# Performance work log

Measured on AMD Instinct MI355X. Metric: run time of the kernel, lower is better.

## Reference

```python
import jax, jax.numpy as jnp
import numpy as np

EPS = 1e-6

def _exp_map0(v):
    # v: [..., D] tangent at origin with v[...,0]==0
    sp = v[..., 1:]
    n = jnp.sqrt(jnp.clip(jnp.sum(sp * sp, -1, keepdims=True), EPS))
    return jnp.concatenate([jnp.cosh(n), jnp.sinh(n) / n * sp], -1)

def _log_map0(x):
    x0 = x[..., :1]
    sp = x[..., 1:]
    n = jnp.sqrt(jnp.clip(jnp.sum(sp * sp, -1, keepdims=True), EPS))
    d = jnp.arccosh(jnp.clip(x0, 1.0 + EPS))
    return jnp.concatenate([jnp.zeros_like(x0), d / n * sp], -1)

def _pt_to_origin(x, v):
    # parallel transport v from T_x to T_o, o=(1,0,...,0):
    # PT(v) = v + <o,v>_L / (1 - <x,o>_L) * (x + o);  <o,v>_L=-v0, <x,o>_L=-x0
    coef = -v[..., :1] / (1.0 + x[..., :1])
    x_plus_o = jnp.concatenate([x[..., :1] + 1.0, x[..., 1:]], -1)
    return v + coef * x_plus_o

def _linear(h, W, b):
    # torch nn.Linear: h @ W.T + b, W: [out, in]
    return jnp.einsum('bne,de->bnd', h, W) + b

def setup_inputs() -> dict:
    key = jax.random.key(0)
    ks = jax.random.split(key, 8)
    B, N, d = 8, 2048, 256
    # manifold points via exp_map0 of small tangents
    t = jax.random.normal(ks[0], (B, N, d), jnp.float32) * 0.1
    x = _exp_map0(jnp.pad(t, ((0, 0), (0, 0), (1, 0))))
    # tangent velocity at x: project random u onto T_x (add <x,u>_L * x since <x,x>_L=-1)
    u = jax.random.normal(ks[1], (B, N, d + 1), jnp.float32) * 0.1
    xu = jnp.sum(x * u, -1, keepdims=True) - 2.0 * x[..., :1] * u[..., :1]  # Lorentz inner
    x_vel = u + xu * x
    s = 1.0 / np.sqrt(d)
    Wq = jax.random.normal(ks[2], (d, d), jnp.float32) * s
    Wk = jax.random.normal(ks[3], (d, d), jnp.float32) * s
    Wv = jax.random.normal(ks[4], (d, d), jnp.float32) * s
    bq = jnp.zeros((d,), jnp.float32)
    bk = jnp.zeros((d,), jnp.float32)
    bv = jnp.zeros((d,), jnp.float32)
    tau = jnp.ones((1,), jnp.float32)
    return {"x": x, "x_vel": x_vel, "Wq": Wq, "bq": bq, "Wk": Wk, "bk": bk,
            "Wv": Wv, "bv": bv, "tau": tau}

def reference(x, x_vel, Wq, bq, Wk, bk, Wv, bv, tau):
    lambda_penalty = 1.0
    log_x = _log_map0(x)
    x_tan = log_x[..., 1:]                                   # [B,N,d]
    q_s = _linear(x_tan, Wq, bq)
    k_s = _linear(x_tan, Wk, bk)
    v_s = _linear(x_tan, Wv, bv)
    pad = lambda h: jnp.pad(h, ((0, 0), (0, 0), (1, 0)))
    q = _exp_map0(pad(q_s))                                  # [B,N,D]
    k = _exp_map0(pad(k_s))
    log_v = pad(v_s)
    vel0 = _pt_to_origin(x, x_vel)
    q_vel = _linear(vel0[..., 1:], Wq, bq)                   # [B,N,d]
    k_vel = _linear(vel0[..., 1:], Wk, bk)
    # pairwise Lorentz distance: <q,k>_L = sum(q*k) - 2*q0*k0
    inner = jnp.einsum('bnd,bmd->bnm', q, k) \
            - 2.0 * q[..., 0][:, :, None] * k[..., 0][:, None, :]
    d_L = jnp.arccosh(jnp.clip(-inner, 1.0 + EPS))           # [B,N,N]
    q_sq = jnp.sum(q_vel * q_vel, -1)                        # [B,N]
    k_sq = jnp.sum(k_vel * k_vel, -1)
    qk = jnp.einsum('bnd,bmd->bnm', q_vel, k_vel)
    pen = jnp.clip(q_sq[:, :, None] + k_sq[:, None, :] - 2.0 * qk, 0.0)
    tau_c = jnp.clip(tau, 0.001)[0]
    logits = -(1.0 / tau_c) * d_L ** 2 - lambda_penalty * pen
    attn = jax.nn.softmax(logits, axis=-1)                   # [B,N,N]
    agg = jnp.einsum('bnm,bmd->bnd', attn, log_v)
    z = _exp_map0(agg)
    return z, attn, x_tan
```

## Files before the change

### kernel.cpp

```cpp
#include <hip/hip_runtime.h>
#include <math.h>

#define BB 8
#define NN 2048
#define DD 256
#define TT (BB*NN)
#define DP1 257
#define EPSF 1e-6f

typedef _Float16 f16;
typedef __attribute__((ext_vector_type(8))) _Float16 f16x8;
typedef __attribute__((ext_vector_type(4))) float f32x4;

#define BAR() asm volatile("s_barrier" ::: "memory")
#define WAIT_VM(N) asm volatile("s_waitcnt vmcnt(" #N ")" ::: "memory")
#define WAIT_LGKM0() asm volatile("s_waitcnt lgkmcnt(0)" ::: "memory")

__device__ __forceinline__ f32x4 mfma16(f16x8 a, f16x8 b, f32x4 c) {
  return __builtin_amdgcn_mfma_f32_16x16x32_f16(a, b, c, 0, 0, 0);
}
__device__ __forceinline__ void gll16(const f16* g, f16* l) {
  __builtin_amdgcn_global_load_lds(
      (const __attribute__((address_space(1))) void*)g,
      (__attribute__((address_space(3))) void*)l, 16, 0, 0);
}

__device__ __forceinline__ float wave_sum(float v) {
#pragma unroll
  for (int m = 1; m < 64; m <<= 1) v += __shfl_xor(v, m);
  return v;
}

__global__ __launch_bounds__(256) void prep_kernel(
    const float* __restrict__ x, const float* __restrict__ xv,
    float* __restrict__ xtan, f16* __restrict__ xtan_h, f16* __restrict__ vel0_h) {
  const int w = threadIdx.x >> 6, l = threadIdx.x & 63;
  const int tok = blockIdx.x * 4 + w;
  const float* xr = x  + (size_t)tok * DP1;
  const float* vr = xv + (size_t)tok * DP1;
  float x0 = xr[0];
  float sp[4];
  float ss = 0.f;
#pragma unroll
  for (int j = 0; j < 4; j++) { sp[j] = xr[1 + l + 64 * j]; ss = fmaf(sp[j], sp[j], ss); }
  ss = wave_sum(ss);
  float n  = sqrtf(fmaxf(ss, EPSF));
  float dd = acoshf(fmaxf(x0, 1.f + EPSF));
  float scl = dd / n;
  float coef = -vr[0] / (1.f + x0);
  const size_t base = (size_t)tok * DD;
#pragma unroll
  for (int j = 0; j < 4; j++) {
    float xt = scl * sp[j];
    xtan[base + l + 64 * j] = xt;
    xtan_h[base + l + 64 * j] = (f16)xt;
    vel0_h[base + l + 64 * j] = (f16)(vr[1 + l + 64 * j] + coef * sp[j]);
  }
}

__global__ __launch_bounds__(256) void wcast_kernel(
    const float* __restrict__ Wq, const float* __restrict__ Wk,
    const float* __restrict__ Wv, f16* __restrict__ Wh) {
  const int m = blockIdx.y;
  const int i = blockIdx.x * 256 + threadIdx.x;
  const float* W = (m == 0) ? Wq : ((m == 1) ? Wk : Wv);
  Wh[(size_t)m * DD * DD + i] = (f16)W[i];
}

__global__ __launch_bounds__(256, 2) void gemm_mfma(
    const f16* __restrict__ xtan_h, const f16* __restrict__ vel0_h,
    const f16* __restrict__ Wh,
    f16* __restrict__ qh, f16* __restrict__ kh, f16* __restrict__ vT,
    f16* __restrict__ qvh, f16* __restrict__ kvh,
    const float* __restrict__ bq, const float* __restrict__ bk,
    const float* __restrict__ bv) {
  __shared__ __align__(16) f16 sA[3 * 4096];
  __shared__ __align__(16) f16 sB[3 * 4096];
  const int tid = threadIdx.x;
  const int bm = blockIdx.x * 128;
  const int bn = blockIdx.y * 128;
  const int seg = bn >> 8;
  const int w = tid >> 6, l = tid & 63;
  const int wr = w >> 1, wc = w & 1;
  f32x4 acc[4][4] = {};
  const f16* Ab = ((seg < 3) ? xtan_h : vel0_h) + (size_t)bm * DD;
  const f16* Bb = Wh + (size_t)((seg < 3) ? bn : (bn - 768)) * DD;

  auto stage = [&](int nx, int buf) {
    const int k0 = nx * 32;
#pragma unroll
    for (int p = 0; p < 2; p++) {
      int u = tid + p * 256;
      int row = u >> 2;
      int q = (u & 3) ^ ((u >> 3) & 3);
      size_t go = (size_t)row * DD + k0 + q * 8;
      size_t lb = (size_t)buf * 4096 + (size_t)(w * 64 + p * 256) * 8;
      gll16(Ab + go, sA + lb);
      gll16(Bb + go, sB + lb);
    }
  };

  stage(0, 0);
  stage(1, 1);
  const int fq = ((l >> 4) ^ ((l >> 1) & 3)) * 8;
  for (int kt = 0; kt < 8; ++kt) {
    if (kt < 6)      { stage(kt + 2, (kt + 2) % 3); WAIT_VM(8); }
    else if (kt == 6){ WAIT_VM(4); }
    else             { WAIT_VM(0); }
    BAR();
    const int co = (kt % 3) * 4096;
    f16x8 af[4], bf[4];
#pragma unroll
    for (int i = 0; i < 4; i++)
      af[i] = *(const f16x8*)(sA + co + (wr * 64 + i * 16 + (l & 15)) * 32 + fq);
#pragma unroll
    for (int j = 0; j < 4; j++)
      bf[j] = *(const f16x8*)(sB + co + (wc * 64 + j * 16 + (l & 15)) * 32 + fq);
    __builtin_amdgcn_s_setprio(1);
#pragma unroll
    for (int i = 0; i < 4; i++)
#pragma unroll
      for (int j = 0; j < 4; j++)
        acc[i][j] = mfma16(af[i], bf[j], acc[i][j]);
    __builtin_amdgcn_s_setprio(0);
    BAR();
  }

  f16* optr = (seg == 0) ? qh : (seg == 1) ? kh : (seg == 2) ? vT : (seg == 3) ? qvh : kvh;
  const float* bias = (seg == 0 || seg == 3) ? bq : (seg == 1 || seg == 4) ? bk : bv;
  const int ot = (seg == 2) ? 1 : 0;
  const int rl = (l >> 4) * 4, cl = l & 15;
#pragma unroll
  for (int i = 0; i < 4; i++) {
#pragma unroll
    for (int j = 0; j < 4; j++) {
      const int col = (bn & 255) + wc * 64 + j * 16 + cl;
      const float bvv = bias[col];
      const int row0 = bm + wr * 64 + i * 16 + rl;
      if (ot == 0) {
#pragma unroll
        for (int r = 0; r < 4; r++)
          optr[(size_t)(row0 + r) * DD + col] = (f16)(acc[i][j][r] + bvv);
      } else {
        __align__(8) f16 tmp[4];
#pragma unroll
        for (int r = 0; r < 4; r++) tmp[r] = (f16)(acc[i][j][r] + bvv);
        f16* dst = optr + ((size_t)((row0 >> 11) * DD + col)) * NN + (row0 & (NN - 1));
        *(uint2*)dst = *(const uint2*)tmp;
      }
    }
  }
}

__global__ __launch_bounds__(256) void norms_kernel(
    const f16* __restrict__ qh, const f16* __restrict__ kh,
    const f16* __restrict__ qvh, const f16* __restrict__ kvh,
    float* __restrict__ q0, float* __restrict__ k0v,
    float* __restrict__ q_sq, float* __restrict__ k_sq,
    float* __restrict__ snq, float* __restrict__ snk) {
  const int w = threadIdx.x >> 6, l = threadIdx.x & 63;
  const int tok = blockIdx.x * 4 + w;
  const size_t base = (size_t)tok * DD;
  float sq = 0.f, sk = 0.f, svq = 0.f, svk = 0.f;
#pragma unroll
  for (int j = 0; j < 4; j++) {
    size_t off = base + l + 64 * j;
    float q = (float)qh[off], k = (float)kh[off];
    float qv = (float)qvh[off], kv = (float)kvh[off];
    sq = fmaf(q, q, sq);
    sk = fmaf(k, k, sk);
    svq = fmaf(qv, qv, svq);
    svk = fmaf(kv, kv, svk);
  }
  sq = wave_sum(sq); sk = wave_sum(sk);
  svq = wave_sum(svq); svk = wave_sum(svk);
  if (l == 0) {
    float nq = sqrtf(fmaxf(sq, EPSF));
    float nk = sqrtf(fmaxf(sk, EPSF));
    q0[tok] = coshf(nq);
    k0v[tok] = coshf(nk);
    q_sq[tok] = svq;
    k_sq[tok] = svk;
    snq[tok] = sinhf(nq) / nq;
    snk[tok] = sinhf(nk) / nk;
  }
}

template<int SF>
__global__ __launch_bounds__(256, 2) void logits_mfma(
    const f16* __restrict__ qh, const f16* __restrict__ kh,
    const f16* __restrict__ qvh, const f16* __restrict__ kvh,
    const float* __restrict__ q0a, const float* __restrict__ k0a,
    const float* __restrict__ qsqa, const float* __restrict__ ksqa,
    const float* __restrict__ snqa, const float* __restrict__ snka,
    const float* __restrict__ tau, float* __restrict__ attn,
    f16* __restrict__ slabh, float* __restrict__ psum) {
  __shared__ __align__(16) f16 sA[3 * 4096];
  __shared__ __align__(16) f16 sB[3 * 4096];
  const int tid = threadIdx.x;
  const int bid = blockIdx.x;
  const int b = bid & 7;
  const int bq = ((bid >> 3) & 15) * 128;
  const int kti = bid >> 7;
  const int bk = kti * 128;
  const size_t tb = (size_t)b * NN;
  const f16* Q  = qh  + (tb + bq) * DD;
  const f16* Kp = kh  + (tb + bk) * DD;
  const f16* Qv = qvh + (tb + bq) * DD;
  const f16* Kv = kvh + (tb + bk) * DD;
  const int w = tid >> 6, l = tid & 63;
  const int wr = w >> 1, wc = w & 1;
  f32x4 accq[4][4] = {}, accv[4][4] = {};
  const int fq = ((l >> 4) ^ ((l >> 1) & 3)) * 8;

  auto stage2 = [&](const f16* Ksrc, const f16* Qsrc, int nx, int buf) {
    const int k0 = nx * 32;
#pragma unroll
    for (int p = 0; p < 2; p++) {
      int u = tid + p * 256;
      int row = u >> 2;
      int q = (u & 3) ^ ((u >> 3) & 3);
      size_t go = (size_t)row * DD + k0 + q * 8;
      size_t lb = (size_t)buf * 4096 + (size_t)(w * 64 + p * 256) * 8;
      gll16(Ksrc + go, sA + lb);
      gll16(Qsrc + go, sB + lb);
    }
  };

#define LMFMA(ACC)                                                              \
  {                                                                             \
    f16x8 ak[4], bqf[4];                                                        \
    _Pragma("unroll")                                                           \
    for (int i = 0; i < 4; i++)                                                 \
      ak[i] = *(const f16x8*)(sA + co + (wr * 64 + i * 16 + (l & 15)) * 32 + fq); \
    _Pragma("unroll")                                                           \
    for (int j = 0; j < 4; j++)                                                 \
      bqf[j] = *(const f16x8*)(sB + co + (wc * 64 + j * 16 + (l & 15)) * 32 + fq); \
    __builtin_amdgcn_s_setprio(1);                                              \
    _Pragma("unroll")                                                           \
    for (int i = 0; i < 4; i++)                                                 \
      _Pragma("unroll")                                                         \
      for (int j = 0; j < 4; j++)                                               \
        ACC[i][j] = mfma16(ak[i], bqf[j], ACC[i][j]);                           \
    __builtin_amdgcn_s_setprio(0);                                              \
  }

  stage2(Kp, Q, 0, 0);
  stage2(Kp, Q, 1, 1);
  for (int kt = 0; kt < 8; ++kt) {
    const int s = kt + 2;
    if (s < 8) stage2(Kp, Q, s, s % 3);
    else       stage2(Kv, Qv, s - 8, s % 3);
    WAIT_VM(8);
    BAR();
    const int co = (kt % 3) * 4096;
    LMFMA(accq)
    BAR();
  }
  for (int kt = 0; kt < 8; ++kt) {
    if (kt < 6)      { stage2(Kv, Qv, kt + 2, (kt + 1) % 3); WAIT_VM(8); }
    else if (kt == 6){ WAIT_VM(4); }
    else             { WAIT_VM(0); }
    BAR();
    const int co = ((kt + 2) % 3) * 4096;
    LMFMA(accv)
    BAR();
  }
#undef LMFMA

  const int rl = (l >> 4) * 4, cl = l & 15;
  const float invt = 1.f / fmaxf(tau[0], 1e-3f);
  const float cc = invt * 0.4804530139182014f;
  float q0r[4], qsr[4], snqr[4];
  float4 k0c[4], ksc[4], snkc[4];
#pragma unroll
  for (int j = 0; j < 4; j++) {
    const int qq = bq + wc * 64 + j * 16 + cl;
    q0r[j] = q0a[tb + qq];
    qsr[j] = qsqa[tb + qq];
    snqr[j] = snqa[tb + qq];
  }
#pragma unroll
  for (int i = 0; i < 4; i++) {
    const int kk = bk + wr * 64 + i * 16 + rl;
    k0c[i] = *(const float4*)(k0a + tb + kk);
    ksc[i] = *(const float4*)(ksqa + tb + kk);
    snkc[i] = *(const float4*)(snka + tb + kk);
  }
  const size_t obase = (size_t)b * NN * NN;
#pragma unroll
  for (int j = 0; j < 4; j++) {
    const int qq = bq + wc * 64 + j * 16 + cl;
    const float q0 = q0r[j], qs = qsr[j], sq = snqr[j];
    float es = 0.f;
#pragma unroll
    for (int i = 0; i < 4; i++) {
      const int kk = bk + wr * 64 + i * 16 + rl;
      const float* k0p = (const float*)&k0c[i];
      const float* ksp = (const float*)&ksc[i];
      const float* skp = (const float*)&snkc[i];
      float4 o;
      float* op = (float*)&o;
      __align__(8) f16 ho[4];
#pragma unroll
      for (int r = 0; r < 4; r++) {
        float sc = sq * skp[r];
        float xv = fmaxf(fmaf(q0, k0p[r], -sc * accq[i][j][r]), 1.f + EPSF);
        float s = sqrtf(fmaf(xv, xv, -1.f));
        float lg = __log2f(xv + s);
        float pen = fmaxf(fmaf(-2.f, accv[i][j][r], qs + ksp[r]), 0.f);
        float lo = fmaf(-cc * lg, lg, -pen);
        float ex = __expf(lo);
        op[r] = ex;
        ho[r] = (f16)ex;
        es += ex;
      }
      if (SF == 1)
        *(uint2*)(slabh + obase + (size_t)qq * NN + kk) = *(const uint2*)ho;
      else
        *(float4*)(attn + obase + (size_t)qq * NN + kk) = o;
    }
    es += __shfl_xor(es, 16);
    es += __shfl_xor(es, 32);
    if ((l >> 4) == 0)
      psum[((size_t)(b * 16 + kti) * 2 + wr) * NN + qq] = es;
  }
}

template<int SF>
__global__ __launch_bounds__(256, 2) void pv_fused(
    const float* __restrict__ psum, const f16* __restrict__ vT,
    const f16* __restrict__ slabh, float* __restrict__ attn, float* __restrict__ z) {
  __shared__ __align__(16) f16 sP[2][32 * 32];
  __shared__ __align__(16) f16 sV[3][256 * 32];
  __shared__ float invs_l[32];
  __shared__ float zsum[4][32];
  __shared__ float zsc[32];
  const int tid = threadIdx.x;
  const int bid = blockIdx.x;
  const int b = bid & 7;
  const int row0 = (bid >> 3) * 32;
  const int w = tid >> 6, l = tid & 63;
  float* slab = attn + ((size_t)b * NN + row0) * NN;
  const f16* slabr = slabh + ((size_t)b * NN + row0) * NN;
  const f16* Vb = vT + (size_t)b * DD * NN;

  if (tid < 32) {
    float s = 0.f;
#pragma unroll 4
    for (int p = 0; p < 32; p++) s += psum[((size_t)b * 32 + p) * NN + row0 + tid];
    invs_l[tid] = 1.f / s;
  }
  __syncthreads();
  const int prow = tid >> 3, pm4 = tid & 7;
  const float myinv = invs_l[prow];
  const int fq = ((l >> 4) ^ ((l >> 1) & 3)) * 8;
  const int spo = prow * 32 + ((pm4 >> 1) ^ ((prow >> 1) & 3)) * 8 + (pm4 & 1) * 4;
  f32x4 acc[2][4] = {};
  float4 pA, pB;

#define STAGEV(nx, vb) do { const int m0_ = (nx) * 32;                          \
    _Pragma("unroll")                                                           \
    for (int p_ = 0; p_ < 4; p_++) {                                            \
      int u_ = tid + p_ * 256;                                                  \
      int d_ = u_ >> 2;                                                         \
      int q_ = (u_ & 3) ^ ((u_ >> 3) & 3);                                      \
      gll16(Vb + (size_t)d_ * NN + m0_ + q_ * 8,                                \
            (f16*)&sV[vb][0] + (size_t)(w * 64 + p_ * 256) * 8);                \
    } } while (0)
#define LOADP(nx, reg) do {                                                     \
    if (SF == 1) {                                                              \
      uint2 rv_ = *(const uint2*)(slabr + (size_t)prow * NN + (nx) * 32 + pm4 * 4); \
      reg.x = __uint_as_float(rv_.x); reg.y = __uint_as_float(rv_.y);           \
    } else {                                                                    \
      reg = *(const float4*)(slab + (size_t)prow * NN + (nx) * 32 + pm4 * 4);   \
    } } while (0)
#define USEP(nx, reg) do {                                                      \
    float e0_, e1_, e2_, e3_;                                                   \
    if (SF == 1) {                                                              \
      uint2 rv_; rv_.x = __float_as_uint(reg.x); rv_.y = __float_as_uint(reg.y);\
      const f16* hp_ = (const f16*)&rv_;                                        \
      e0_ = (float)hp_[0] * myinv; e1_ = (float)hp_[1] * myinv;                 \
      e2_ = (float)hp_[2] * myinv; e3_ = (float)hp_[3] * myinv;                 \
    } else {                                                                    \
      e0_ = reg.x * myinv; e1_ = reg.y * myinv;                                 \
      e2_ = reg.z * myinv; e3_ = reg.w * myinv;                                 \
    }                                                                           \
    float4 ov_ = {e0_, e1_, e2_, e3_};                                          \
    *(float4*)(slab + (size_t)prow * NN + (nx) * 32 + pm4 * 4) = ov_;           \
    __align__(8) f16 tmp_[4] = {(f16)e0_, (f16)e1_, (f16)e2_, (f16)e3_};        \
    *(uint2*)(&sP[(nx) & 1][spo]) = *(const uint2*)tmp_;                        \
  } while (0)
#define COMPUTE(t, vb) do {                                                     \
    f16x8 af_[2], bf_[4];                                                       \
    _Pragma("unroll")                                                           \
    for (int i_ = 0; i_ < 2; i_++)                                              \
      af_[i_] = *(const f16x8*)(&sP[(t) & 1][(i_ * 16 + (l & 15)) * 32 + fq]);  \
    _Pragma("unroll")                                                           \
    for (int j_ = 0; j_ < 4; j_++)                                              \
      bf_[j_] = *(const f16x8*)((const f16*)&sV[vb][0] +                        \
                                (w * 64 + j_ * 16 + (l & 15)) * 32 + fq);       \
    _Pragma("unroll")                                                           \
    for (int i_ = 0; i_ < 2; i_++)                                              \
      _Pragma("unroll")                                                         \
      for (int j_ = 0; j_ < 4; j_++)                                            \
        acc[i_][j_] = mfma16(af_[i_], bf_[j_], acc[i_][j_]);                    \
  } while (0)

  STAGEV(0, 0); LOADP(0, pA);
  STAGEV(1, 1); LOADP(1, pB);
  WAIT_VM(5);
  USEP(0, pA);
  WAIT_LGKM0();
  BAR();

  int vb0 = 0;
  for (int tt = 0; tt < 32; ++tt) {
    {
      const int t = 2 * tt;
      const int vb_t = vb0;
      const int vb_s = (vb0 + 2 > 2) ? vb0 - 1 : vb0 + 2;
      if (t < 62) { STAGEV(t + 2, vb_s); LOADP(t + 2, pA); WAIT_VM(5); }
      else        { WAIT_VM(1); }
      if (t < 63) USEP(t + 1, pB);
      COMPUTE(t, vb_t);
      WAIT_LGKM0();
      BAR();
    }
    {
      const int t = 2 * tt + 1;
      const int vb_t = (vb0 + 1 > 2) ? vb0 - 2 : vb0 + 1;
      const int vb_s = vb0;
      if (t < 62)      { STAGEV(t + 2, vb_s); LOADP(t + 2, pB); WAIT_VM(5); }
      else if (t == 62){ WAIT_VM(1); }
      else             { WAIT_VM(0); }
      if (t < 63) USEP(t + 1, pA);
      COMPUTE(t, vb_t);
      WAIT_LGKM0();
      BAR();
    }
    vb0 = (vb0 + 2 > 2) ? vb0 - 1 : vb0 + 2;
  }
#undef STAGEV
#undef LOADP
#undef USEP
#undef COMPUTE

  const int rl4 = (l >> 4) * 4, cl = l & 15;
  float s2[2][4];
#pragma unroll
  for (int i = 0; i < 2; i++)
#pragma unroll
    for (int r = 0; r < 4; r++) {
      float s = 0.f;
#pragma unroll
      for (int j = 0; j < 4; j++) s = fmaf(acc[i][j][r], acc[i][j][r], s);
#pragma unroll
      for (int m = 1; m < 16; m <<= 1) s += __shfl_xor(s, m);
      s2[i][r] = s;
    }
  if (cl == 0) {
#pragma unroll
    for (int i = 0; i < 2; i++)
#pragma unroll
      for (int r = 0; r < 4; r++)
        zsum[w][i * 16 + rl4 + r] = s2[i][r];
  }
  __syncthreads();
  if (tid < 32) {
    float n2 = zsum[0][tid] + zsum[1][tid] + zsum[2][tid] + zsum[3][tid];
    float nn = sqrtf(fmaxf(n2, EPSF));
    zsc[tid] = sinhf(nn) / nn;
    z[(size_t)(b * NN + row0 + tid) * DP1] = coshf(nn);
  }
  __syncthreads();
#pragma unroll
  for (int i = 0; i < 2; i++)
#pragma unroll
    for (int r = 0; r < 4; r++) {
      const int row = i * 16 + rl4 + r;
      const float sc = zsc[row];
      const size_t zb = (size_t)(b * NN + row0 + row) * DP1 + 1;
#pragma unroll
      for (int j = 0; j < 4; j++)
        z[zb + w * 64 + j * 16 + cl] = acc[i][j][r] * sc;
    }
}

extern "C" void kernel_launch(void* const* d_in, const int* in_sizes, int n_in,
                              void* d_out, int out_size, void* d_ws, size_t ws_size,
                              hipStream_t stream) {
  const float* x   = (const float*)d_in[0];
  const float* xv  = (const float*)d_in[1];
  const float* Wq  = (const float*)d_in[2];
  const float* bq  = (const float*)d_in[3];
  const float* Wk  = (const float*)d_in[4];
  const float* bk  = (const float*)d_in[5];
  const float* Wv  = (const float*)d_in[6];
  const float* bv  = (const float*)d_in[7];
  const float* tau = (const float*)d_in[8];
  float* out = (float*)d_out;
  char* ws = (char*)d_ws;

  const size_t TD2 = (size_t)TT * DD * 2;

  f16*   qh     = (f16*)(ws);
  f16*   kh     = (f16*)(ws + TD2);
  f16*   qvh    = (f16*)(ws + 2 * TD2);
  f16*   kvh    = (f16*)(ws + 3 * TD2);
  f16*   vT     = (f16*)(ws + 4 * TD2);
  f16*   xtan_h = (f16*)(ws + 5 * TD2);
  f16*   vel0_h = (f16*)(ws + 6 * TD2);
  f16*   Wh     = (f16*)(ws + 7 * TD2);
  float* psum   = (float*)(ws + 7 * TD2 + 3 * DD * DD * 2);
  float* q0     = psum + (size_t)BB * 32 * NN;
  float* k0v    = q0 + TT;
  float* q_sq   = q0 + 2 * TT;
  float* k_sq   = q0 + 3 * TT;
  float* snq    = q0 + 4 * TT;
  float* snk    = q0 + 5 * TT;
  const size_t fixed_end = 7 * TD2 + 3 * DD * DD * 2 +
                           ((size_t)BB * 32 * NN + 6 * (size_t)TT) * 4;
  f16* slabh = (f16*)(ws + fixed_end);
  const size_t need = fixed_end + (size_t)BB * NN * NN * 2;
  const bool big_ws = (ws_size >= need);

  float* z_out    = out;
  float* attn_out = out + (size_t)TT * DP1;
  float* xtan_out = attn_out + (size_t)BB * NN * NN;

  prep_kernel<<<TT / 4, 256, 0, stream>>>(x, xv, xtan_out, xtan_h, vel0_h);
  wcast_kernel<<<dim3(DD * DD / 256, 3), 256, 0, stream>>>(Wq, Wk, Wv, Wh);

  gemm_mfma<<<dim3(TT / 128, 10), 256, 0, stream>>>(
      xtan_h, vel0_h, Wh, qh, kh, vT, qvh, kvh, bq, bk, bv);

  norms_kernel<<<TT / 4, 256, 0, stream>>>(qh, kh, qvh, kvh, q0, k0v, q_sq, k_sq, snq, snk);

  if (big_ws) {
    logits_mfma<1><<<NN / 128 * NN / 128 * BB, 256, 0, stream>>>(
        qh, kh, qvh, kvh, q0, k0v, q_sq, k_sq, snq, snk, tau, attn_out, slabh, psum);
    pv_fused<1><<<NN / 32 * BB, 256, 0, stream>>>(psum, vT, slabh, attn_out, z_out);
  } else {
    logits_mfma<0><<<NN / 128 * NN / 128 * BB, 256, 0, stream>>>(
        qh, kh, qvh, kvh, q0, k0v, q_sq, k_sq, snq, snk, tau, attn_out, slabh, psum);
    pv_fused<0><<<NN / 32 * BB, 256, 0, stream>>>(psum, vT, slabh, attn_out, z_out);
  }
}
```

Measured before the change: 186.9 us.

## Enlarge logits tile to 256 keys with 512-thread blocks sharing Q tiles

The logits kernel now uses 512-thread blocks, each covering 128 queries by 256 keys instead of 128x128. Every staged Q slice feeds twice as many K rows, which halves Q reloads from global memory and halves the number of blocks. The K shared buffer doubles, the wait counts and the psum indexing are adjusted to match, and the launch grid shrinks. The trade-off is more LDS per block, which may cut occupancy, and fewer blocks for load balance. The pv kernel has to read psum with the new layout (four partials per 256-key group, eight groups), and that code is not visible here.

```diff
diff --git a/kernel.cpp b/kernel.cpp
--- a/kernel.cpp
+++ b/kernel.cpp
@@ -187,7 +187,7 @@
 }
 
 template<int SF>
-__global__ __launch_bounds__(256, 2) void logits_mfma(
+__global__ __launch_bounds__(512, 2) void logits_mfma(
     const f16* __restrict__ qh, const f16* __restrict__ kh,
     const f16* __restrict__ qvh, const f16* __restrict__ kvh,
     const float* __restrict__ q0a, const float* __restrict__ k0a,
@@ -195,14 +195,14 @@
     const float* __restrict__ snqa, const float* __restrict__ snka,
     const float* __restrict__ tau, float* __restrict__ attn,
     f16* __restrict__ slabh, float* __restrict__ psum) {
-  __shared__ __align__(16) f16 sA[3 * 4096];
+  __shared__ __align__(16) f16 sA[3 * 8192];
   __shared__ __align__(16) f16 sB[3 * 4096];
   const int tid = threadIdx.x;
   const int bid = blockIdx.x;
   const int b = bid & 7;
   const int bq = ((bid >> 3) & 15) * 128;
   const int kti = bid >> 7;
-  const int bk = kti * 128;
+  const int bk = kti * 256;
   const size_t tb = (size_t)b * NN;
   const f16* Q  = qh  + (tb + bq) * DD;
   const f16* Kp = kh  + (tb + bk) * DD;
@@ -217,25 +217,35 @@
     const int k0 = nx * 32;
 #pragma unroll
     for (int p = 0; p < 2; p++) {
-      int u = tid + p * 256;
+      int u = tid + p * 512;
       int row = u >> 2;
       int q = (u & 3) ^ ((u >> 3) & 3);
-      size_t go = (size_t)row * DD + k0 + q * 8;
-      size_t lb = (size_t)buf * 4096 + (size_t)(w * 64 + p * 256) * 8;
-      gll16(Ksrc + go, sA + lb);
-      gll16(Qsrc + go, sB + lb);
+      gll16(Ksrc + (size_t)row * DD + k0 + q * 8,
+            sA + (size_t)buf * 8192 + (size_t)(w * 64 + p * 512) * 8);
+    }
+    {
+      int u = tid;
+      int row = u >> 2;
+      int q = (u & 3) ^ ((u >> 3) & 3);
+      gll16(Qsrc + (size_t)row * DD + k0 + q * 8,
+            sB + (size_t)buf * 4096 + (size_t)(w * 64) * 8);
     }
   };
-
-#define LMFMA(ACC)                                                              \
+  auto stageg = [&](int s) {
+    if (s < 8) stage2(Kp, Q, s, s % 3);
+    else       stage2(Kv, Qv, s - 8, s % 3);
+  };
+
+#define LMFMA(ACC, CO)                                                          \
   {                                                                             \
+    const int coA = (CO) * 8192, coB = (CO) * 4096;                             \
     f16x8 ak[4], bqf[4];                                                        \
     _Pragma("unroll")                                                           \
     for (int i = 0; i < 4; i++)                                                 \
-      ak[i] = *(const f16x8*)(sA + co + (wr * 64 + i * 16 + (l & 15)) * 32 + fq); \
+      ak[i] = *(const f16x8*)(sA + coA + (wr * 64 + i * 16 + (l & 15)) * 32 + fq); \
     _Pragma("unroll")                                                           \
     for (int j = 0; j < 4; j++)                                                 \
-      bqf[j] = *(const f16x8*)(sB + co + (wc * 64 + j * 16 + (l & 15)) * 32 + fq); \
+      bqf[j] = *(const f16x8*)(sB + coB + (wc * 64 + j * 16 + (l & 15)) * 32 + fq); \
     __builtin_amdgcn_s_setprio(1);                                              \
     _Pragma("unroll")                                                           \
     for (int i = 0; i < 4; i++)                                                 \
@@ -245,25 +255,21 @@
     __builtin_amdgcn_s_setprio(0);                                              \
   }
 
-  stage2(Kp, Q, 0, 0);
-  stage2(Kp, Q, 1, 1);
-  for (int kt = 0; kt < 8; ++kt) {
-    const int s = kt + 2;
-    if (s < 8) stage2(Kp, Q, s, s % 3);
-    else       stage2(Kv, Qv, s - 8, s % 3);
-    WAIT_VM(8);
+  stageg(0);
+  stageg(1);
+  for (int g = 0; g < 8; ++g) {
+    stageg(g + 2);
+    WAIT_VM(6);
     BAR();
-    const int co = (kt % 3) * 4096;
-    LMFMA(accq)
+    LMFMA(accq, g % 3)
     BAR();
   }
-  for (int kt = 0; kt < 8; ++kt) {
-    if (kt < 6)      { stage2(Kv, Qv, kt + 2, (kt + 1) % 3); WAIT_VM(8); }
-    else if (kt == 6){ WAIT_VM(4); }
-    else             { WAIT_VM(0); }
+  for (int h = 0; h < 8; ++h) {
+    if (h < 6)      { stageg(h + 10); WAIT_VM(6); }
+    else if (h == 6){ WAIT_VM(3); }
+    else            { WAIT_VM(0); }
     BAR();
-    const int co = ((kt + 2) % 3) * 4096;
-    LMFMA(accv)
+    LMFMA(accv, (h + 2) % 3)
     BAR();
   }
 #undef LMFMA
@@ -323,7 +329,7 @@
     es += __shfl_xor(es, 16);
     es += __shfl_xor(es, 32);
     if ((l >> 4) == 0)
-      psum[((size_t)(b * 16 + kti) * 2 + wr) * NN + qq] = es;
+      psum[((size_t)((b * 8 + kti) * 4 + wr)) * NN + qq] = es;
   }
 }
 
@@ -375,7 +381,7 @@
     } else {                                                                    \
       reg = *(const float4*)(slab + (size_t)prow * NN + (nx) * 32 + pm4 * 4);   \
     } } while (0)
-#define USEP(nx, reg) do {                                                      \
+#define USEP(nx, reg) do {                                                     \
     float e0_, e1_, e2_, e3_;                                                   \
     if (SF == 1) {                                                              \
       uint2 rv_; rv_.x = __float_as_uint(reg.x); rv_.y = __float_as_uint(reg.y);\
@@ -538,11 +544,11 @@
   norms_kernel<<<TT / 4, 256, 0, stream>>>(qh, kh, qvh, kvh, q0, k0v, q_sq, k_sq, snq, snk);
 
   if (big_ws) {
-    logits_mfma<1><<<NN / 128 * NN / 128 * BB, 256, 0, stream>>>(
+    logits_mfma<1><<<NN / 256 * NN / 128 * BB, 512, 0, stream>>>(
         qh, kh, qvh, kvh, q0, k0v, q_sq, k_sq, snq, snk, tau, attn_out, slabh, psum);
     pv_fused<1><<<NN / 32 * BB, 256, 0, stream>>>(psum, vT, slabh, attn_out, z_out);
   } else {
-    logits_mfma<0><<<NN / 128 * NN / 128 * BB, 256, 0, stream>>>(
+    logits_mfma<0><<<NN / 256 * NN / 128 * BB, 512, 0, stream>>>(
         qh, kh, qvh, kvh, q0, k0v, q_sq, k_sq, snq, snk, tau, attn_out, slabh, psum);
     pv_fused<0><<<NN / 32 * BB, 256, 0, stream>>>(psum, vT, slabh, attn_out, z_out);
   }
```

Measured after the change: 196.5 us. 1.05x slower.
